# Kernel tuning notes

Hardware: AMD Instinct MI355X
Metric: run time of the kernel (lower is better)

## Reference

```python
import jax, jax.numpy as jnp
import numpy as np

B, T, E, H, FF = 8, 1024, 1024, 16, 4096
HD = E // H
SCALE = HD ** -0.5
EPS = 1e-12  # LayerNorm eps from TransformerLayer


def layer_norm(x, w, b):
    u = x.mean(-1, keepdims=True)
    s = ((x - u) ** 2).mean(-1, keepdims=True)  # biased variance, as in module
    return w * (x - u) / jnp.sqrt(s + EPS) + b


def setup_inputs() -> dict:
    key = jax.random.key(0)
    ks = jax.random.split(key, 8)
    std = 0.02  # nn.init.normal_(std=0.02)
    x = jax.random.normal(ks[0], (B, T, E), jnp.float32)
    # padding mask: positions >= length are padding (1 = ignore); ensure no all-masked row
    lengths = jax.random.randint(ks[1], (B,), T // 2, T + 1)
    self_padding_mask = jnp.arange(T)[None, :] >= lengths[:, None]
    # causal mask from SelfAttentionMask: triu(ones, 1)
    attn_mask = jnp.triu(jnp.ones((T, T), dtype=bool), 1)
    in_w = std * jax.random.normal(ks[2], (3 * E, E), jnp.float32)
    in_b = jnp.zeros((3 * E,), jnp.float32)
    out_w = std * jax.random.normal(ks[3], (E, E), jnp.float32)
    out_b = jnp.zeros((E,), jnp.float32)
    fc1_w = std * jax.random.normal(ks[4], (FF, E), jnp.float32)
    fc1_b = jnp.zeros((FF,), jnp.float32)
    fc2_w = std * jax.random.normal(ks[5], (E, FF), jnp.float32)
    fc2_b = jnp.zeros((E,), jnp.float32)
    ln1_w = jnp.ones((E,), jnp.float32)
    ln1_b = jnp.zeros((E,), jnp.float32)
    ln2_w = jnp.ones((E,), jnp.float32)
    ln2_b = jnp.zeros((E,), jnp.float32)
    return dict(x=x, in_w=in_w, in_b=in_b, out_w=out_w, out_b=out_b,
                fc1_w=fc1_w, fc1_b=fc1_b, fc2_w=fc2_w, fc2_b=fc2_b,
                ln1_w=ln1_w, ln1_b=ln1_b, ln2_w=ln2_w, ln2_b=ln2_b,
                self_padding_mask=self_padding_mask, attn_mask=attn_mask)


def reference(x, in_w, in_b, out_w, out_b, fc1_w, fc1_b, fc2_w, fc2_b,
              ln1_w, ln1_b, ln2_w, ln2_b, self_padding_mask, attn_mask):
    b, t, e = x.shape
    # --- self attention sublayer ---
    residual = x
    qkv = x @ in_w.T + in_b                       # [B,T,3E] fused in_proj (qkv_same path)
    q, k, v = jnp.split(qkv, 3, axis=-1)
    q = (q * SCALE).reshape(b, t, H, HD)
    k = k.reshape(b, t, H, HD)
    v = v.reshape(b, t, H, HD)
    scores = jnp.einsum('bqhd,bkhd->bhqk', q, k)  # [B,H,T,T]
    mask = attn_mask[None, None, :, :] | self_padding_mask[:, None, None, :]
    scores = jnp.where(mask, -jnp.inf, scores)
    p = jax.nn.softmax(scores, axis=-1)
    attn = jnp.einsum('bhqk,bkhd->bqhd', p, v).reshape(b, t, e)
    attn = attn @ out_w.T + out_b
    x = layer_norm(residual + attn, ln1_w, ln1_b)
    # --- feed-forward sublayer ---
    residual = x
    h = jax.nn.relu(x @ fc1_w.T + fc1_b)
    x = layer_norm(residual + (h @ fc2_w.T + fc2_b), ln2_w, ln2_b)
    return x
```

## Files before the change

kernel.cpp:

```cpp
#include <hip/hip_runtime.h>

typedef unsigned short u16;
typedef __attribute__((ext_vector_type(8))) short short8;
typedef __attribute__((ext_vector_type(4))) short short4v;
typedef __attribute__((ext_vector_type(4))) float f32x4;

#define DEV static __device__ __forceinline__

DEV float bf2f(u16 h) {
    union { unsigned int u; float f; } v; v.u = ((unsigned int)h) << 16; return v.f;
}
DEV u16 f2bf(float f) {
    union { float f; unsigned int u; } v; v.f = f;
    unsigned int r = (v.u + 0x7fff + ((v.u >> 16) & 1)) >> 16;
    return (u16)r;
}
DEV float ldx(const void* p, size_t i, int f32) {
    return f32 ? ((const float*)p)[i] : bf2f(((const u16*)p)[i]);
}

#define QSCL 0.18033688011112042f

#define GLD16(g, l) __builtin_amdgcn_global_load_lds( \
    (const __attribute__((address_space(1))) void*)(g), \
    (__attribute__((address_space(3))) void*)(l), 16, 0, 0)

#define STAGE(P, pf32, eoff, dst8) do {                                        \
    if (!(pf32)) { GLD16(((const u16*)(P)) + (eoff), (dst8)); }                \
    else {                                                                     \
        const float* _p = ((const float*)(P)) + (eoff);                        \
        f32x4 _a = *(const f32x4*)_p, _b = *(const f32x4*)(_p + 4);            \
        short8 _s;                                                             \
        _s[0]=(short)f2bf(_a[0]); _s[1]=(short)f2bf(_a[1]);                    \
        _s[2]=(short)f2bf(_a[2]); _s[3]=(short)f2bf(_a[3]);                    \
        _s[4]=(short)f2bf(_b[0]); _s[5]=(short)f2bf(_b[1]);                    \
        _s[6]=(short)f2bf(_b[2]); _s[7]=(short)f2bf(_b[3]);                    \
        *(short8*)(dst8) = _s;                                                 \
    } } while (0)

__global__ __launch_bounds__(64) void probe_kernel(
    const void* __restrict__ x, const void* __restrict__ pad,
    int* __restrict__ flags, int* __restrict__ flagsA)
{
    const int lane = threadIdx.x;
    const u16* xu = (const u16*)x;
    const unsigned int e = (xu[lane * 2] >> 7) & 0xFF;
    const int sane = (e >= 0x70 && e <= 0x8F) ? 1 : 0;
    unsigned long long m = __ballot(sane);
    const int f32 = (__popcll(m) < 32) ? 1 : 0;

    const unsigned int* pi = (const unsigned int*)pad;
    int bytes = 0;
#pragma unroll
    for (int j = 0; j < 6; j++) {
        unsigned int v = pi[128 + j * 64 + lane];
        if (v > 1u) bytes = 1;
    }
    m = __ballot(bytes);
    if (lane == 0) {
        flags[0] = f32; flags[1] = (m != 0ULL) ? 1 : 0;
        flagsA[0] = 0;  flagsA[1] = 0;
    }
}

__global__ __launch_bounds__(256) void conv8(
    const void* __restrict__ src, u16* __restrict__ dst, int n8,
    const int* __restrict__ flags)
{
    const int i = blockIdx.x * 256 + threadIdx.x;
    if (i >= n8) return;
    if (flags[0]) {
        const float* p = (const float*)src + (size_t)i * 8;
        f32x4 a = *(const f32x4*)p, b = *(const f32x4*)(p + 4);
        short8 s;
        s[0]=(short)f2bf(a[0]); s[1]=(short)f2bf(a[1]);
        s[2]=(short)f2bf(a[2]); s[3]=(short)f2bf(a[3]);
        s[4]=(short)f2bf(b[0]); s[5]=(short)f2bf(b[1]);
        s[6]=(short)f2bf(b[2]); s[7]=(short)f2bf(b[3]);
        ((short8*)dst)[i] = s;
    } else {
        ((short8*)dst)[i] = ((const short8*)src)[i];
    }
}

__global__ __launch_bounds__(256) void mask_to_bias(
    const void* __restrict__ pad, float* __restrict__ out,
    const int* __restrict__ flags)
{
    const int i = blockIdx.x * 256 + threadIdx.x;
    const int mv = flags[1] ? (int)((const unsigned char*)pad)[i]
                            : ((const int*)pad)[i];
    out[i] = mv ? -1e30f : 0.0f;
}

#define GEMM_CORE(Av, ASEL, a_row0, Wv, w_off, ldw, K)                        \
    __shared__ __align__(16) u16 As[128 * 32];                                \
    __shared__ __align__(16) u16 Bs[128 * 32];                                \
    const int inf32 = flags[0];                                               \
    const int af32  = (ASEL) ? inf32 : 0;                                     \
    const int tid  = threadIdx.x;                                             \
    const int lane = tid & 63;                                                \
    const int wave = tid >> 6;                                                \
    const int lc   = lane & 15;                                               \
    const int quad = lane >> 4;                                               \
    const int m0 = blockIdx.x * 128;                                          \
    const int n0 = blockIdx.y * 128;                                          \
    const int wm = (wave >> 1) * 64;                                          \
    const int wn = (wave & 1) * 64;                                           \
    const int r0 = tid >> 2;                                                  \
    const int ko = (tid & 3) * 8;                                             \
    f32x4 acc[4][4] = {};                                                     \
    for (int k0 = 0; k0 < (K); k0 += 32) {                                    \
        STAGE(Av, af32, ((size_t)(a_row0) + m0 + r0) * (K) + k0 + ko,         \
              &As[tid * 8]);                                                  \
        STAGE(Av, af32, ((size_t)(a_row0) + m0 + r0 + 64) * (K) + k0 + ko,    \
              &As[2048 + tid * 8]);                                           \
        STAGE(Wv, inf32, (size_t)(w_off) + (size_t)(n0 + r0) * (ldw) + k0 + ko,\
              &Bs[tid * 8]);                                                  \
        STAGE(Wv, inf32, (size_t)(w_off) + (size_t)(n0 + r0 + 64) * (ldw) + k0 + ko,\
              &Bs[2048 + tid * 8]);                                           \
        __syncthreads();                                                      \
        short8 afr[4], bfr[4];                                                \
        const int qd = quad * 8;                                              \
        _Pragma("unroll")                                                     \
        for (int mt = 0; mt < 4; mt++)                                        \
            afr[mt] = *(const short8*)&As[(wm + mt * 16 + lc) * 32 + qd];     \
        _Pragma("unroll")                                                     \
        for (int nt = 0; nt < 4; nt++)                                        \
            bfr[nt] = *(const short8*)&Bs[(wn + nt * 16 + lc) * 32 + qd];     \
        _Pragma("unroll")                                                     \
        for (int mt = 0; mt < 4; mt++)                                        \
            _Pragma("unroll")                                                 \
            for (int nt = 0; nt < 4; nt++)                                    \
                acc[mt][nt] = __builtin_amdgcn_mfma_f32_16x16x32_bf16(        \
                    afr[mt], bfr[nt], acc[mt][nt], 0, 0, 0);                  \
        __syncthreads();                                                      \
    }                                                                         \
    const int ce0 = n0 + wn + lc;                                             \
    const int re0 = m0 + wm + quad * 4;

template<int EPI>
__global__ __launch_bounds__(256, 2) void gemm_bt(
    const void* __restrict__ A, int a_sel, long a_row0,
    const void* __restrict__ W, long w_off,
    const void* __restrict__ bias, long b_off,
    const void* __restrict__ resid, int r_sel, long r_row0,
    u16* __restrict__ C, long c_row0,
    int N, int K, int ldw, const int* __restrict__ flags)
{
    GEMM_CORE(A, a_sel, a_row0, W, w_off, ldw, K)
    const int rf32 = r_sel ? inf32 : 0;
#pragma unroll
    for (int mt = 0; mt < 4; mt++) {
#pragma unroll
        for (int nt = 0; nt < 4; nt++) {
            const int c = ce0 + nt * 16;
            const float bv = ldx(bias, (size_t)b_off + c, inf32);
#pragma unroll
            for (int i = 0; i < 4; i++) {
                const int r = re0 + mt * 16 + i;
                float v = acc[mt][nt][i] + bv;
                if (EPI == 1)
                    v += ldx(resid, ((size_t)r_row0 + r) * N + c, rf32);
                if (EPI == 2) v = fmaxf(v, 0.0f);
                C[((size_t)c_row0 + r) * N + c] = f2bf(v);
            }
        }
    }
}

__global__ __launch_bounds__(256, 2) void gemm_qkv(
    const void* __restrict__ A, long a_row0,
    const void* __restrict__ W, const void* __restrict__ bias,
    u16* __restrict__ Qo, u16* __restrict__ Ko, u16* __restrict__ Vt,
    const int* __restrict__ flags)
{
    GEMM_CORE(A, 1, a_row0, W, 0, 1024, 1024)
    if (n0 < 1024) {
#pragma unroll
        for (int mt = 0; mt < 4; mt++)
#pragma unroll
            for (int nt = 0; nt < 4; nt++) {
                const int c = ce0 + nt * 16;
                const float bv = ldx(bias, c, inf32);
#pragma unroll
                for (int i = 0; i < 4; i++) {
                    const int r = re0 + mt * 16 + i;
                    Qo[((size_t)a_row0 + r) * 1024 + c] =
                        f2bf((acc[mt][nt][i] + bv) * QSCL);
                }
            }
    } else if (n0 < 2048) {
#pragma unroll
        for (int mt = 0; mt < 4; mt++)
#pragma unroll
            for (int nt = 0; nt < 4; nt++) {
                const int c = ce0 + nt * 16;
                const float bv = ldx(bias, c, inf32);
#pragma unroll
                for (int i = 0; i < 4; i++) {
                    const int r = re0 + mt * 16 + i;
                    Ko[(size_t)r * 1024 + (c - 1024)] = f2bf(acc[mt][nt][i] + bv);
                }
            }
    } else {
#pragma unroll
        for (int mt = 0; mt < 4; mt++)
#pragma unroll
            for (int nt = 0; nt < 4; nt++) {
                const int c = ce0 + nt * 16;
                const float bv = ldx(bias, c, inf32);
                const int cv = c - 2048;
                const int hh = cv >> 6, d = cv & 63;
                const int rb = re0 + mt * 16;
                const int bl = rb >> 10, t = rb & 1023;
                short4v pk;
#pragma unroll
                for (int i = 0; i < 4; i++)
                    pk[i] = (short)f2bf(acc[mt][nt][i] + bv);
                *(short4v*)&Vt[((size_t)(bl * 16 + hh) * 64 + d) * 1024 + t] = pk;
            }
    }
}

__global__ __launch_bounds__(256, 2) void gemm_accf32(
    const void* __restrict__ A, const void* __restrict__ W, long w_off,
    const void* __restrict__ bias, const u16* __restrict__ resid, long r_row0,
    float* __restrict__ C, int ldw, int init, const int* __restrict__ flags)
{
    GEMM_CORE(A, 0, 0, W, w_off, ldw, 1024)
#pragma unroll
    for (int mt = 0; mt < 4; mt++) {
#pragma unroll
        for (int nt = 0; nt < 4; nt++) {
            const int c = ce0 + nt * 16;
            const float bv = ldx(bias, c, inf32);
#pragma unroll
            for (int i = 0; i < 4; i++) {
                const int r = re0 + mt * 16 + i;
                float v = acc[mt][nt][i];
                if (init) v += bv + bf2f(resid[((size_t)r_row0 + r) * 1024 + c]);
                else      v += C[(size_t)r * 1024 + c];
                C[(size_t)r * 1024 + c] = v;
            }
        }
    }
}

#define GEMM8_PRE(Ag_, Wg_, Kg_)                                              \
    __shared__ __align__(16) u16 Ab[3][128 * 64];                             \
    __shared__ __align__(16) u16 Bb[3][256 * 64];                             \
    const u16* Ag = (Ag_); const u16* Wg = (Wg_); const int Kg = (Kg_);       \
    const int tid  = threadIdx.x;                                             \
    const int lane = tid & 63;                                                \
    const int lc   = lane & 15;                                               \
    const int quad = lane >> 4;                                               \
    const int w    = tid >> 6;                                                \
    const int wr   = w >> 2;                                                  \
    const int wc   = w & 3;                                                   \
    const int m0 = blockIdx.x * 128;                                          \
    const int n0 = blockIdx.y * 256;                                          \
    const int srow = tid >> 3;                                                \
    const int scol = (((tid & 7) ^ (srow & 7)) << 3);                         \
    const int sw0 = (((quad) ^ (lc & 7)) << 3);                               \
    const int sw1 = sw0 ^ 32;                                                 \
    f32x4 acc[4][4] = {};                                                     \
    short8 af[4], bf[4];

#define SA8(buf, kk) do {                                                     \
    GLD16(Ag + (size_t)(m0 + srow) * Kg + (kk) + scol, &Ab[buf][tid * 8]);    \
    GLD16(Ag + (size_t)(m0 + 64 + srow) * Kg + (kk) + scol,                   \
          &Ab[buf][4096 + tid * 8]); } while (0)
#define SB8a(buf, kk) do {                                                    \
    GLD16(Wg + (size_t)(n0 + srow) * Kg + (kk) + scol, &Bb[buf][tid * 8]);    \
    GLD16(Wg + (size_t)(n0 + 64 + srow) * Kg + (kk) + scol,                   \
          &Bb[buf][4096 + tid * 8]); } while (0)
#define SB8b(buf, kk) do {                                                    \
    GLD16(Wg + (size_t)(n0 + 128 + srow) * Kg + (kk) + scol,                  \
          &Bb[buf][8192 + tid * 8]);                                          \
    GLD16(Wg + (size_t)(n0 + 192 + srow) * Kg + (kk) + scol,                  \
          &Bb[buf][12288 + tid * 8]); } while (0)
#define LDFR(rbuf, SW) do { _Pragma("unroll")                                 \
    for (int q_ = 0; q_ < 4; q_++) {                                          \
        af[q_] = *(const short8*)&Ab[rbuf][(wr * 64 + q_ * 16 + lc) * 64 + (SW)];\
        bf[q_] = *(const short8*)&Bb[rbuf][(wc * 64 + q_ * 16 + lc) * 64 + (SW)];\
    } } while (0)
#define MFMA16 do { _Pragma("unroll")                                         \
    for (int mq = 0; mq < 4; mq++) { _Pragma("unroll")                        \
    for (int nq = 0; nq < 4; nq++)                                            \
        acc[mq][nq] = __builtin_amdgcn_mfma_f32_16x16x32_bf16(                \
            af[mq], bf[nq], acc[mq][nq], 0, 0, 0); } } while (0)

#define GEMM8_LOOP                                                            \
    const int NT = Kg >> 6;                                                   \
    SA8(0, 0); SB8a(0, 0); SB8b(0, 0);                                        \
    if (NT > 1) { SA8(1, 64); SB8a(1, 64); SB8b(1, 64); }                     \
    if (NT > 1) asm volatile("s_waitcnt vmcnt(6)" ::: "memory");              \
    else        asm volatile("s_waitcnt vmcnt(0)" ::: "memory");              \
    __builtin_amdgcn_s_barrier();                                             \
    int rb_ = 0, wb_ = 2;                                                     \
    for (int t = 0; t < NT; ++t) {                                            \
        const bool s_ = (t + 2 < NT);                                         \
        const int k2_ = (t + 2) << 6;                                         \
        LDFR(rb_, sw0);                                                       \
        if (s_) { SA8(wb_, k2_); SB8a(wb_, k2_); }                            \
        __builtin_amdgcn_s_barrier();                                         \
        asm volatile("s_waitcnt lgkmcnt(0)" ::: "memory");                    \
        __builtin_amdgcn_s_setprio(1);                                        \
        MFMA16;                                                               \
        __builtin_amdgcn_s_setprio(0);                                        \
        __builtin_amdgcn_s_barrier();                                         \
        LDFR(rb_, sw1);                                                       \
        if (s_) SB8b(wb_, k2_);                                               \
        __builtin_amdgcn_s_barrier();                                         \
        asm volatile("s_waitcnt lgkmcnt(0)" ::: "memory");                    \
        __builtin_amdgcn_s_setprio(1);                                        \
        MFMA16;                                                               \
        __builtin_amdgcn_s_setprio(0);                                        \
        if (s_) asm volatile("s_waitcnt vmcnt(6)" ::: "memory");              \
        else    asm volatile("s_waitcnt vmcnt(0)" ::: "memory");              \
        __builtin_amdgcn_s_barrier();                                         \
        rb_ = (rb_ == 2) ? 0 : rb_ + 1;                                      \
        wb_ = (wb_ == 2) ? 0 : wb_ + 1;                                      \
    }                                                                         \
    const int cb0 = n0 + wc * 64 + lc;                                        \
    const int rb0 = m0 + wr * 64 + quad * 4;

template<int EPI>
__global__ __launch_bounds__(512, 2) void gemm8(
    const u16* __restrict__ A, const u16* __restrict__ W,
    const u16* __restrict__ bias, const u16* __restrict__ resid,
    u16* __restrict__ C, int N, int K)
{
    GEMM8_PRE(A, W, K)
    GEMM8_LOOP
#pragma unroll
    for (int mq = 0; mq < 4; mq++) {
#pragma unroll
        for (int nq = 0; nq < 4; nq++) {
            const int cN = cb0 + nq * 16;
            const float bv = bf2f(bias[cN]);
#pragma unroll
            for (int i = 0; i < 4; i++) {
                const int rM = rb0 + mq * 16 + i;
                float v = acc[mq][nq][i] + bv;
                if (EPI == 1) v += bf2f(resid[(size_t)rM * N + cN]);
                if (EPI == 2) v = fmaxf(v, 0.0f);
                C[(size_t)rM * N + cN] = f2bf(v);
            }
        }
    }
}

__global__ __launch_bounds__(512, 2) void gemm8_qkv(
    const u16* __restrict__ A, const u16* __restrict__ W,
    const u16* __restrict__ bias,
    u16* __restrict__ Qo, u16* __restrict__ Ko, u16* __restrict__ Vt)
{
    GEMM8_PRE(A, W, 1024)
    GEMM8_LOOP
    if (n0 < 1024) {
#pragma unroll
        for (int mq = 0; mq < 4; mq++)
#pragma unroll
            for (int nq = 0; nq < 4; nq++) {
                const int c = cb0 + nq * 16;
                const float bv = bf2f(bias[c]);
#pragma unroll
                for (int i = 0; i < 4; i++) {
                    const int r = rb0 + mq * 16 + i;
                    Qo[(size_t)r * 1024 + c] =
                        f2bf((acc[mq][nq][i] + bv) * QSCL);
                }
            }
    } else if (n0 < 2048) {
#pragma unroll
        for (int mq = 0; mq < 4; mq++)
#pragma unroll
            for (int nq = 0; nq < 4; nq++) {
                const int c = cb0 + nq * 16;
                const float bv = bf2f(bias[c]);
#pragma unroll
                for (int i = 0; i < 4; i++) {
                    const int r = rb0 + mq * 16 + i;
                    Ko[(size_t)r * 1024 + (c - 1024)] =
                        f2bf(acc[mq][nq][i] + bv);
                }
            }
    } else {
#pragma unroll
        for (int mq = 0; mq < 4; mq++)
#pragma unroll
            for (int nq = 0; nq < 4; nq++) {
                const int c = cb0 + nq * 16;
                const float bv = bf2f(bias[c]);
                const int cv = c - 2048;
                const int hh = cv >> 6, d = cv & 63;
                const int rbase = rb0 + mq * 16;
                const int bl = rbase >> 10, tt = rbase & 1023;
                short4v pk;
#pragma unroll
                for (int i = 0; i < 4; i++)
                    pk[i] = (short)f2bf(acc[mq][nq][i] + bv);
                *(short4v*)&Vt[((size_t)(bl * 16 + hh) * 64 + d) * 1024 + tt] = pk;
            }
    }
}

#define GEMM256_PRE(Ag_, Wg_, Kg_)                                            \
    __shared__ __align__(16) u16 Ab2[2][2][8192];                             \
    __shared__ __align__(16) u16 Bb2[2][2][8192];                             \
    const u16* Ag = (Ag_); const u16* Wg = (Wg_); const int Kg = (Kg_);       \
    const int tid  = threadIdx.x;                                             \
    const int lane = tid & 63;                                                \
    const int lc   = lane & 15;                                               \
    const int quad = lane >> 4;                                               \
    const int w    = tid >> 6;                                                \
    const int wr   = w >> 2;                                                  \
    const int wc   = w & 3;                                                   \
    const int m0 = blockIdx.x * 256;                                          \
    const int n0 = blockIdx.y * 256;                                          \
    const int s_r = tid >> 2;                                                 \
    const int s_c = (((tid & 3) ^ ((tid >> 3) & 3)) << 3);                    \
    const int fsw = ((quad ^ ((lc >> 1) & 3)) << 3);                          \
    const int arow = wr * 128 + lc;                                           \
    const int brow = wc * 64 + lc;                                            \
    f32x4 acc[8][4] = {};                                                     \
    short8 af[4], bf[4];

#define SAH(buf, kk, tt) do {                                                 \
    GLD16(Ag + (size_t)(m0 + s_r) * Kg + (tt) * 64 + (kk) * 32 + s_c,         \
          &Ab2[buf][kk][tid * 8]);                                            \
    GLD16(Ag + (size_t)(m0 + 128 + s_r) * Kg + (tt) * 64 + (kk) * 32 + s_c,   \
          &Ab2[buf][kk][4096 + tid * 8]); } while (0)
#define SBH(buf, kk, tt) do {                                                 \
    GLD16(Wg + (size_t)(n0 + s_r) * Kg + (tt) * 64 + (kk) * 32 + s_c,         \
          &Bb2[buf][kk][tid * 8]);                                            \
    GLD16(Wg + (size_t)(n0 + 128 + s_r) * Kg + (tt) * 64 + (kk) * 32 + s_c,   \
          &Bb2[buf][kk][4096 + tid * 8]); } while (0)
#define LDA2(buf, kk, MH) do { _Pragma("unroll")                              \
    for (int q_ = 0; q_ < 4; q_++)                                            \
        af[q_] = *(const short8*)                                             \
            &Ab2[buf][kk][(arow + ((MH) * 4 + q_) * 16) * 32 + fsw]; } while (0)
#define LDB2(buf, kk) do { _Pragma("unroll")                                  \
    for (int q_ = 0; q_ < 4; q_++)                                            \
        bf[q_] = *(const short8*)                                             \
            &Bb2[buf][kk][(brow + q_ * 16) * 32 + fsw]; } while (0)
#define MF256(MH) do { _Pragma("unroll")                                      \
    for (int mq = 0; mq < 4; mq++) { _Pragma("unroll")                        \
    for (int nq = 0; nq < 4; nq++)                                            \
        acc[(MH) * 4 + mq][nq] = __builtin_amdgcn_mfma_f32_16x16x32_bf16(     \
            af[mq], bf[nq], acc[(MH) * 4 + mq][nq], 0, 0, 0); } } while (0)

#define GEMM256_LOOP                                                          \
    const int NT = Kg >> 6;                                                   \
    SAH(0, 0, 0); SBH(0, 0, 0); SAH(0, 1, 0); SBH(0, 1, 0);                   \
    if (NT > 1) SAH(1, 0, 1);                                                 \
    if (NT > 1) asm volatile("s_waitcnt vmcnt(2)" ::: "memory");              \
    else        asm volatile("s_waitcnt vmcnt(0)" ::: "memory");              \
    __builtin_amdgcn_s_barrier();                                             \
    for (int t = 0; t < NT; ++t) {                                            \
        const int c_ = t & 1, nx_ = c_ ^ 1;                                   \
        const bool s1_ = (t + 1 < NT), s2_ = (t + 2 < NT);                    \
                                                          \
        LDB2(c_, 0); LDA2(c_, 0, 0);                                          \
        if (s1_) SBH(nx_, 0, t + 1);                                          \
        __builtin_amdgcn_s_barrier();                                         \
        asm volatile("s_waitcnt lgkmcnt(0)" ::: "memory");                    \
        __builtin_amdgcn_s_setprio(1);                                        \
        MF256(0);                                                             \
        __builtin_amdgcn_s_setprio(0);                                        \
        __builtin_amdgcn_s_barrier();                                         \
                                         \
        LDA2(c_, 0, 1);                                                       \
        if (s1_) SAH(nx_, 1, t + 1);                                          \
        __builtin_amdgcn_s_barrier();                                         \
        asm volatile("s_waitcnt lgkmcnt(0)" ::: "memory");                    \
        __builtin_amdgcn_s_setprio(1);                                        \
        MF256(1);                                                             \
        __builtin_amdgcn_s_setprio(0);                                        \
        if (s1_) asm volatile("s_waitcnt vmcnt(6)" ::: "memory");             \
        else     asm volatile("s_waitcnt vmcnt(0)" ::: "memory");             \
        __builtin_amdgcn_s_barrier();                                         \
                                                          \
        LDB2(c_, 1); LDA2(c_, 1, 0);                                          \
        if (s1_) SBH(nx_, 1, t + 1);                                          \
        __builtin_amdgcn_s_barrier();                                         \
        asm volatile("s_waitcnt lgkmcnt(0)" ::: "memory");                    \
        __builtin_amdgcn_s_setprio(1);                                        \
        MF256(0);                                                             \
        __builtin_amdgcn_s_setprio(0);                                        \
        __builtin_amdgcn_s_barrier();                                         \
                \
        LDA2(c_, 1, 1);                                                       \
        if (s2_) SAH(c_, 0, t + 2);                                           \
        __builtin_amdgcn_s_barrier();                                         \
        asm volatile("s_waitcnt lgkmcnt(0)" ::: "memory");                    \
        __builtin_amdgcn_s_setprio(1);                                        \
        MF256(1);                                                             \
        __builtin_amdgcn_s_setprio(0);                                        \
        if (s2_)      asm volatile("s_waitcnt vmcnt(6)" ::: "memory");        \
        else if (s1_) asm volatile("s_waitcnt vmcnt(4)" ::: "memory");        \
        else          asm volatile("s_waitcnt vmcnt(0)" ::: "memory");        \
        __builtin_amdgcn_s_barrier();                                         \
    }                                                                         \
    const int cb0 = n0 + wc * 64 + lc;                                        \
    const int rb0 = m0 + wr * 128 + quad * 4;

template<int EPI>
__global__ __launch_bounds__(512, 2) void gemm256(
    const u16* __restrict__ A, const u16* __restrict__ W,
    const u16* __restrict__ bias, const u16* __restrict__ resid,
    u16* __restrict__ C, int N, int K)
{
    GEMM256_PRE(A, W, K)
    GEMM256_LOOP
#pragma unroll
    for (int mq = 0; mq < 8; mq++) {
#pragma unroll
        for (int nq = 0; nq < 4; nq++) {
            const int cN = cb0 + nq * 16;
            const float bv = bf2f(bias[cN]);
#pragma unroll
            for (int i = 0; i < 4; i++) {
                const int rM = rb0 + mq * 16 + i;
                float v = acc[mq][nq][i] + bv;
                if (EPI == 1) v += bf2f(resid[(size_t)rM * N + cN]);
                if (EPI == 2) v = fmaxf(v, 0.0f);
                C[(size_t)rM * N + cN] = f2bf(v);
            }
        }
    }
}

__global__ __launch_bounds__(256, 2) void attn_kernel(
    u16* __restrict__ QO, const u16* __restrict__ Ko,
    const u16* __restrict__ Vt, const float* __restrict__ kb, int b0)
{
    __shared__ __align__(16) u16 Qs[2 * 128 * 32];
    __shared__ __align__(16) u16 Ks[2][2 * 64 * 32];
    __shared__ __align__(16) u16 Vs[2][2 * 64 * 32];
    __shared__ __align__(16) u16 Ps[4][32 * 72];
    __shared__ float kba[1024];

    const int tid  = threadIdx.x;
    const int lane = tid & 63;
    const int w    = tid >> 6;
    const int lc   = lane & 15;
    const int quad = lane >> 4;
    const int bl = blockIdx.y >> 4;
    const int h  = blockIdx.y & 15;
    const int b  = b0 + bl;

    short8 bsum;
    {
        const short ov = (lc == 0) ? (short)0x3F80 : (short)0;
#pragma unroll
        for (int j = 0; j < 8; j++) bsum[j] = ov;
    }

    *(f32x4*)&kba[tid * 4] = *(const f32x4*)&kb[b * 1024 + tid * 4];

    for (int p = 0; p < 2; p++) {
        const int qt = p ? 7 - (int)blockIdx.x : (int)blockIdx.x;

#pragma unroll
        for (int it = 0; it < 4; it++) {
            const int kcd = it >> 1, half = it & 1;
            const int r = half * 64 + (tid >> 2);
            const int c = kcd * 32 + (tid & 3) * 8;
            GLD16(&QO[((size_t)(b * 1024 + qt * 128 + r)) * 1024 + h * 64 + c],
                  &Qs[kcd * 4096 + half * 2048 + tid * 8]);
        }
        {
            const int rr = tid >> 2;
#pragma unroll
            for (int it = 0; it < 2; it++) {
                const int cc = it * 32 + (tid & 3) * 8;
                GLD16(&Ko[((size_t)(bl * 1024 + rr)) * 1024 + h * 64 + cc],
                      &Ks[0][it * 2048 + tid * 8]);
                GLD16(&Vt[((size_t)(bl * 16 + h) * 64 + rr) * 1024 + cc],
                      &Vs[0][it * 2048 + tid * 8]);
            }
        }
        __syncthreads();

        short8 aq[2][2];
#pragma unroll
        for (int mt = 0; mt < 2; mt++)
#pragma unroll
            for (int kc = 0; kc < 2; kc++)
                aq[mt][kc] = *(const short8*)
                    &Qs[kc * 4096 + (w * 32 + mt * 16 + lc) * 32 + quad * 8];

        f32x4 o[2][4] = {};
        float m_i[2][4], l_i[2][4];
#pragma unroll
        for (int mt = 0; mt < 2; mt++)
#pragma unroll
            for (int i = 0; i < 4; i++) { m_i[mt][i] = -1e30f; l_i[mt][i] = 0.0f; }

        const int ktmax = 2 * qt + 2;
        for (int kt = 0; kt < ktmax; kt++) {
            const int cur = kt & 1;
            if (kt + 1 < ktmax) {
                const int nxt = cur ^ 1;
                const int rr = tid >> 2;
#pragma unroll
                for (int it = 0; it < 2; it++) {
                    const int cc = it * 32 + (tid & 3) * 8;
                    GLD16(&Ko[((size_t)(bl * 1024 + (kt + 1) * 64 + rr)) * 1024 + h * 64 + cc],
                          &Ks[nxt][it * 2048 + tid * 8]);
                    GLD16(&Vt[((size_t)(bl * 16 + h) * 64 + rr) * 1024 + (kt + 1) * 64 + cc],
                          &Vs[nxt][it * 2048 + tid * 8]);
                }
            }

            short8 bk[4][2];
#pragma unroll
            for (int nt = 0; nt < 4; nt++)
#pragma unroll
                for (int kc = 0; kc < 2; kc++)
                    bk[nt][kc] = *(const short8*)
                        &Ks[cur][kc * 2048 + (nt * 16 + lc) * 32 + quad * 8];

            f32x4 s[2][4];
#pragma unroll
            for (int mt = 0; mt < 2; mt++)
#pragma unroll
                for (int nt = 0; nt < 4; nt++) {
                    f32x4 z = {};
#pragma unroll
                    for (int kc = 0; kc < 2; kc++)
                        z = __builtin_amdgcn_mfma_f32_16x16x32_bf16(
                            aq[mt][kc], bk[nt][kc], z, 0, 0, 0);
                    s[mt][nt] = z;
                }

#pragma unroll
            for (int mt = 0; mt < 2; mt++)
#pragma unroll
                for (int nt = 0; nt < 4; nt++) {
                    const float kbv = kba[kt * 64 + nt * 16 + lc];
#pragma unroll
                    for (int i = 0; i < 4; i++) s[mt][nt][i] += kbv;
                }
            if (kt >= 2 * qt) {
#pragma unroll
                for (int mt = 0; mt < 2; mt++) {
                    const int qg0 = qt * 128 + w * 32 + mt * 16 + quad * 4;
#pragma unroll
                    for (int nt = 0; nt < 4; nt++) {
                        const int kg = kt * 64 + nt * 16 + lc;
#pragma unroll
                        for (int i = 0; i < 4; i++)
                            if (kg > qg0 + i) s[mt][nt][i] = -1e30f;
                    }
                }
            }

            float al[2][4];
#pragma unroll
            for (int mt = 0; mt < 2; mt++) {
                float mnew[4];
#pragma unroll
                for (int i = 0; i < 4; i++) {
                    float rm = fmaxf(fmaxf(s[mt][0][i], s[mt][1][i]),
                                     fmaxf(s[mt][2][i], s[mt][3][i]));
                    rm = fmaxf(rm, __shfl_xor(rm, 1));
                    rm = fmaxf(rm, __shfl_xor(rm, 2));
                    rm = fmaxf(rm, __shfl_xor(rm, 4));
                    rm = fmaxf(rm, __shfl_xor(rm, 8));
                    const float mn = fmaxf(m_i[mt][i], rm);
                    al[mt][i] = exp2f(m_i[mt][i] - mn);
                    m_i[mt][i] = mn;
                    mnew[i] = mn;
                }
#pragma unroll
                for (int nt = 0; nt < 4; nt++)
#pragma unroll
                    for (int i = 0; i < 4; i++)
                        s[mt][nt][i] = exp2f(s[mt][nt][i] - mnew[i]);
#pragma unroll
                for (int nt = 0; nt < 4; nt++) {
#pragma unroll
                    for (int i2 = 0; i2 < 2; i2++) {
                        unsigned int pk;
                        asm("v_cvt_pk_bf16_f32 %0, %1, %2"
                            : "=v"(pk)
                            : "v"(s[mt][nt][2 * i2]), "v"(s[mt][nt][2 * i2 + 1]));
                        Ps[w][(mt * 16 + quad * 4 + 2 * i2) * 72 + nt * 16 + lc] =
                            (u16)pk;
                        Ps[w][(mt * 16 + quad * 4 + 2 * i2 + 1) * 72 + nt * 16 + lc] =
                            (u16)(pk >> 16);
                    }
                }
            }
            int chg = 0;
#pragma unroll
            for (int mt = 0; mt < 2; mt++)
#pragma unroll
                for (int i = 0; i < 4; i++)
                    chg |= (al[mt][i] != 1.0f) ? 1 : 0;
            const int dor = __any(chg);

            short8 ap[2][2], bv2[4][2];
#pragma unroll
            for (int mt = 0; mt < 2; mt++)
#pragma unroll
                for (int kc = 0; kc < 2; kc++)
                    ap[mt][kc] = *(const short8*)
                        &Ps[w][(mt * 16 + lc) * 72 + kc * 32 + quad * 8];
#pragma unroll
            for (int nt = 0; nt < 4; nt++)
#pragma unroll
                for (int kc = 0; kc < 2; kc++)
                    bv2[nt][kc] = *(const short8*)
                        &Vs[cur][kc * 2048 + (nt * 16 + lc) * 32 + quad * 8];

            f32x4 ls[2] = {};
#pragma unroll
            for (int mt = 0; mt < 2; mt++)
#pragma unroll
                for (int kc = 0; kc < 2; kc++)
                    ls[mt] = __builtin_amdgcn_mfma_f32_16x16x32_bf16(
                        ap[mt][kc], bsum, ls[mt], 0, 0, 0);

#pragma unroll
            for (int mt = 0; mt < 2; mt++)
#pragma unroll
                for (int nt = 0; nt < 4; nt++) {
                    f32x4 oo = o[mt][nt];
                    if (dor) {
#pragma unroll
                        for (int i = 0; i < 4; i++) oo[i] *= al[mt][i];
                    }
#pragma unroll
                    for (int kc = 0; kc < 2; kc++)
                        oo = __builtin_amdgcn_mfma_f32_16x16x32_bf16(
                            ap[mt][kc], bv2[nt][kc], oo, 0, 0, 0);
                    o[mt][nt] = oo;
                }
#pragma unroll
            for (int mt = 0; mt < 2; mt++)
#pragma unroll
                for (int i = 0; i < 4; i++)
                    l_i[mt][i] = l_i[mt][i] * al[mt][i] + ls[mt][i];

            __syncthreads();
        }

#pragma unroll
        for (int mt = 0; mt < 2; mt++)
#pragma unroll
            for (int i = 0; i < 4; i++) {
                const float lv = __shfl(l_i[mt][i], (lane & 48));
                const float inv = lv > 0.0f ? 1.0f / lv : 0.0f;
#pragma unroll
                for (int nt = 0; nt < 4; nt++) {
                    const int r = qt * 128 + w * 32 + mt * 16 + quad * 4 + i;
                    const int d = nt * 16 + lc;
                    QO[((size_t)(b * 1024 + r)) * 1024 + h * 64 + d] =
                        f2bf(o[mt][nt][i] * inv);
                }
            }
    }
}

template<int IN16, int OUTSEL>
__global__ __launch_bounds__(256) void ln_kernel(
    const void* __restrict__ yv, const void* __restrict__ w,
    const void* __restrict__ bb, void* __restrict__ o, long o_row0,
    const int* __restrict__ flags)
{
    const int row = blockIdx.x;
    const int tid = threadIdx.x;
    const int inf32 = flags[0];
    float x0, x1, x2, x3;
    if (IN16) {
        const u16* p = (const u16*)yv + (size_t)row * 1024 + tid * 4;
        short4v v = *(const short4v*)p;
        x0 = bf2f((u16)v[0]); x1 = bf2f((u16)v[1]);
        x2 = bf2f((u16)v[2]); x3 = bf2f((u16)v[3]);
    } else {
        const float* p = (const float*)yv + (size_t)row * 1024 + tid * 4;
        f32x4 v = *(const f32x4*)p;
        x0 = v[0]; x1 = v[1]; x2 = v[2]; x3 = v[3];
    }
    float s = x0 + x1 + x2 + x3;
    float q = x0 * x0 + x1 * x1 + x2 * x2 + x3 * x3;
#pragma unroll
    for (int off = 32; off; off >>= 1) {
        s += __shfl_xor(s, off);
        q += __shfl_xor(q, off);
    }
    __shared__ float sm[8];
    const int lane = tid & 63, wv = tid >> 6;
    if (lane == 0) { sm[wv] = s; sm[4 + wv] = q; }
    __syncthreads();
    const float ts = sm[0] + sm[1] + sm[2] + sm[3];
    const float tq = sm[4] + sm[5] + sm[6] + sm[7];
    const float mean = ts * (1.0f / 1024.0f);
    float var = tq * (1.0f / 1024.0f) - mean * mean;
    if (var < 0.0f) var = 0.0f;
    const float rinv = rsqrtf(var + 1e-12f);

    const size_t obase = ((size_t)o_row0 + row) * 1024 + tid * 4;
#pragma unroll
    for (int j = 0; j < 4; j++) {
        const int c = tid * 4 + j;
        float xv = (j == 0) ? x0 : (j == 1) ? x1 : (j == 2) ? x2 : x3;
        float v = ldx(w, c, inf32) * ((xv - mean) * rinv) + ldx(bb, c, inf32);
        if (OUTSEL && inf32) ((float*)o)[obase + j] = v;
        else                 ((u16*)o)[obase + j] = f2bf(v);
    }
}

extern "C" void kernel_launch(void* const* d_in, const int* in_sizes, int n_in,
                              void* d_out, int out_size, void* d_ws, size_t ws_size,
                              hipStream_t stream)
{
    const void* x     = d_in[0];
    const void* in_w  = d_in[1];
    const void* in_b  = d_in[2];
    const void* out_w = d_in[3];
    const void* out_b = d_in[4];
    const void* fc1_w = d_in[5];
    const void* fc1_b = d_in[6];
    const void* fc2_w = d_in[7];
    const void* fc2_b = d_in[8];
    const void* ln1w  = d_in[9];
    const void* ln1b  = d_in[10];
    const void* ln2w  = d_in[11];
    const void* ln2b  = d_in[12];
    const void* pad   = d_in[13];
    u16* outp = (u16*)d_out;
    char* ws = (char*)d_ws;
    dim3 blk(256);
    dim3 blk8(512);

    const size_t MB = 1024 * 1024;
    const bool bigWS = ws_size >= (105 * MB + 64 * 1024);

    if (bigWS) {
        u16*   xb   = (u16*)(ws + 0);
        u16*   x1   = (u16*)(ws + 0);
        u16*   w1b  = (u16*)(ws + 16 * MB);
        u16*   wob  = (u16*)(ws + 22 * MB);
        u16*   f1b  = (u16*)(ws + 24 * MB);
        u16*   f2b  = (u16*)(ws + 32 * MB);
        u16*   inbb = (u16*)(ws + 40 * MB);
        u16*   outbb= (u16*)(ws + 40 * MB + 8192);
        u16*   f1bb = (u16*)(ws + 40 * MB + 16384);
        u16*   f2bb = (u16*)(ws + 40 * MB + 24576);
        u16*   Ko   = (u16*)(ws + 41 * MB);
        u16*   Vt   = (u16*)(ws + 57 * MB);
        u16*   y1   = (u16*)(ws + 73 * MB);
        u16*   h    = (u16*)(ws + 41 * MB);
        u16*   y2   = (u16*)(ws + 16 * MB);
        int*   flags  = (int*)(ws + 105 * MB);
        int*   flagsA = (int*)(ws + 105 * MB + 32);
        float* kbias  = (float*)(ws + 105 * MB + 64);

        probe_kernel<<<dim3(1), dim3(64), 0, stream>>>(x, pad, flags, flagsA);
        mask_to_bias<<<dim3(32), blk, 0, stream>>>(pad, kbias, flags);
        conv8<<<dim3(4096), blk, 0, stream>>>(x, xb, 1048576, flags);
        conv8<<<dim3(1536), blk, 0, stream>>>(in_w, w1b, 393216, flags);
        conv8<<<dim3(512),  blk, 0, stream>>>(out_w, wob, 131072, flags);
        conv8<<<dim3(2048), blk, 0, stream>>>(fc1_w, f1b, 524288, flags);
        conv8<<<dim3(2048), blk, 0, stream>>>(fc2_w, f2b, 524288, flags);
        conv8<<<dim3(2), blk, 0, stream>>>(in_b, inbb, 384, flags);
        conv8<<<dim3(1), blk, 0, stream>>>(out_b, outbb, 128, flags);
        conv8<<<dim3(2), blk, 0, stream>>>(fc1_b, f1bb, 512, flags);
        conv8<<<dim3(1), blk, 0, stream>>>(fc2_b, f2bb, 128, flags);

        gemm8_qkv<<<dim3(64, 12), blk8, 0, stream>>>(
            xb, w1b, inbb, outp, Ko, Vt);
        attn_kernel<<<dim3(4, 128), blk, 0, stream>>>(outp, Ko, Vt, kbias, 0);
        gemm8<1><<<dim3(64, 4), blk8, 0, stream>>>(
            outp, wob, outbb, xb, y1, 1024, 1024);
        ln_kernel<1, 0><<<dim3(8192), blk, 0, stream>>>(y1, ln1w, ln1b, x1, 0, flags);
        gemm256<2><<<dim3(32, 16), blk8, 0, stream>>>(
            x1, f1b, f1bb, nullptr, h, 4096, 1024);
        gemm8<1><<<dim3(64, 4), blk8, 0, stream>>>(
            h, f2b, f2bb, x1, y2, 1024, 4096);
        ln_kernel<1, 1><<<dim3(8192), blk, 0, stream>>>(y2, ln2w, ln2b, d_out, 0, flags);
    } else {
        u16*   Ko    = (u16*)(ws + 0);
        u16*   Vt    = (u16*)(ws + 4 * MB);
        u16*   y1h   = (u16*)(ws + 0);
        float* acc   = (float*)(ws + 0);
        u16*   hc    = (u16*)(ws + 8 * MB);
        int*   flags  = (int*)(ws + 12 * MB);
        int*   flagsA = (int*)(ws + 12 * MB + 32);
        float* kbias  = (float*)(ws + 12 * MB + 64);

        probe_kernel<<<dim3(1), dim3(64), 0, stream>>>(x, pad, flags, flagsA);
        mask_to_bias<<<dim3(32), blk, 0, stream>>>(pad, kbias, flags);

        for (int q = 0; q < 4; q++) {
            const long r0 = (long)q * 2048;
            gemm_qkv<<<dim3(16, 24), blk, 0, stream>>>(
                x, r0, in_w, in_b, outp, Ko, Vt, flags);
            attn_kernel<<<dim3(4, 32), blk, 0, stream>>>(
                outp, Ko, Vt, kbias, q * 2);
        }
        for (int hf = 0; hf < 2; hf++) {
            const long r0 = (long)hf * 4096;
            gemm_bt<1><<<dim3(32, 8), blk, 0, stream>>>(
                outp, 0, r0, out_w, 0, out_b, 0, x, 1, r0,
                y1h, 0, 1024, 1024, 1024, flags);
            ln_kernel<1, 0><<<dim3(4096), blk, 0, stream>>>(
                y1h, ln1w, ln1b, outp, r0, flags);
        }
        for (int q = 3; q >= 0; q--) {
            const long r0 = (long)q * 2048;
            for (int c = 0; c < 4; c++) {
                gemm_bt<2><<<dim3(16, 8), blk, 0, stream>>>(
                    outp, 0, r0, fc1_w, (long)c * 1024 * 1024, fc1_b, (long)c * 1024,
                    nullptr, 0, 0, hc, 0, 1024, 1024, 1024, flags);
                gemm_accf32<<<dim3(16, 8), blk, 0, stream>>>(
                    hc, fc2_w, (long)c * 1024, fc2_b, outp, r0,
                    acc, 4096, c == 0, flags);
            }
            ln_kernel<0, 1><<<dim3(2048), blk, 0, stream>>>(
                acc, ln2w, ln2b, d_out, r0, flags);
        }
    }
}
```

Before: 512.6 us.

## Fuse conversion launches and restructure gemm256 loop with fewer barriers

Nine separate conversion launches (input, weights, biases) are merged into one kernel that picks its source and destination by global index, which removes launch overhead. The gemm256 main loop now loads all A/B fragments for a K-tile up front into larger register arrays and interleaves global prefetches between MFMA groups. This cuts the per-tile barriers and lgkmcnt waits from about eight to two. The cost is higher register pressure from holding 24 short8 fragments, which may lower occupancy at launch_bounds(512,2). Dropping the intermediate barriers and explicit LDS waits also makes correct synchronisation depend on the compiler inserting the waits.

```diff
diff --git a/kernel.cpp b/kernel.cpp
--- a/kernel.cpp
+++ b/kernel.cpp
@@ -63,23 +63,40 @@
     }
 }
 
-__global__ __launch_bounds__(256) void conv8(
-    const void* __restrict__ src, u16* __restrict__ dst, int n8,
+__global__ __launch_bounds__(256) void conv_all(
+    const void* __restrict__ x, const void* __restrict__ in_w,
+    const void* __restrict__ out_w, const void* __restrict__ fc1_w,
+    const void* __restrict__ fc2_w, const void* __restrict__ in_b,
+    const void* __restrict__ out_b, const void* __restrict__ fc1_b,
+    const void* __restrict__ fc2_b,
+    u16* __restrict__ xb, u16* __restrict__ w1b, u16* __restrict__ wob,
+    u16* __restrict__ f1b, u16* __restrict__ f2b, u16* __restrict__ inbb,
+    u16* __restrict__ outbb, u16* __restrict__ f1bb, u16* __restrict__ f2bb,
     const int* __restrict__ flags)
 {
-    const int i = blockIdx.x * 256 + threadIdx.x;
-    if (i >= n8) return;
+    const size_t i = (size_t)blockIdx.x * 256 + threadIdx.x;
+    const void* src; u16* dst; size_t off;
+    if      (i < 1048576u) { src = x;     dst = xb;    off = i; }
+    else if (i < 1441792u) { src = in_w;  dst = w1b;   off = i - 1048576u; }
+    else if (i < 1572864u) { src = out_w; dst = wob;   off = i - 1441792u; }
+    else if (i < 2097152u) { src = fc1_w; dst = f1b;   off = i - 1572864u; }
+    else if (i < 2621440u) { src = fc2_w; dst = f2b;   off = i - 2097152u; }
+    else if (i < 2621824u) { src = in_b;  dst = inbb;  off = i - 2621440u; }
+    else if (i < 2621952u) { src = out_b; dst = outbb; off = i - 2621824u; }
+    else if (i < 2622464u) { src = fc1_b; dst = f1bb;  off = i - 2621952u; }
+    else if (i < 2622592u) { src = fc2_b; dst = f2bb;  off = i - 2622464u; }
+    else return;
     if (flags[0]) {
-        const float* p = (const float*)src + (size_t)i * 8;
+        const float* p = (const float*)src + off * 8;
         f32x4 a = *(const f32x4*)p, b = *(const f32x4*)(p + 4);
         short8 s;
         s[0]=(short)f2bf(a[0]); s[1]=(short)f2bf(a[1]);
         s[2]=(short)f2bf(a[2]); s[3]=(short)f2bf(a[3]);
         s[4]=(short)f2bf(b[0]); s[5]=(short)f2bf(b[1]);
         s[6]=(short)f2bf(b[2]); s[7]=(short)f2bf(b[3]);
-        ((short8*)dst)[i] = s;
+        ((short8*)dst)[off] = s;
     } else {
-        ((short8*)dst)[i] = ((const short8*)src)[i];
+        ((short8*)dst)[off] = ((const short8*)src)[off];
     }
 }
 
@@ -426,7 +443,8 @@
     const int arow = wr * 128 + lc;                                           \
     const int brow = wc * 64 + lc;                                            \
     f32x4 acc[8][4] = {};                                                     \
-    short8 af[4], bf[4];
+    short8 afx[4][4];                                                         \
+    short8 bfx[2][4];
 
 #define SAH(buf, kk, tt) do {                                                 \
     GLD16(Ag + (size_t)(m0 + s_r) * Kg + (tt) * 64 + (kk) * 32 + s_c,         \
@@ -438,19 +456,19 @@
           &Bb2[buf][kk][tid * 8]);                                            \
     GLD16(Wg + (size_t)(n0 + 128 + s_r) * Kg + (tt) * 64 + (kk) * 32 + s_c,   \
           &Bb2[buf][kk][4096 + tid * 8]); } while (0)
-#define LDA2(buf, kk, MH) do { _Pragma("unroll")                              \
+#define LDA3(DST, buf, kk, MH) do { _Pragma("unroll")                         \
     for (int q_ = 0; q_ < 4; q_++)                                            \
-        af[q_] = *(const short8*)                                             \
+        afx[DST][q_] = *(const short8*)                                       \
             &Ab2[buf][kk][(arow + ((MH) * 4 + q_) * 16) * 32 + fsw]; } while (0)
-#define LDB2(buf, kk) do { _Pragma("unroll")                                  \
+#define LDB3(DST, buf, kk) do { _Pragma("unroll")                             \
     for (int q_ = 0; q_ < 4; q_++)                                            \
-        bf[q_] = *(const short8*)                                             \
+        bfx[DST][q_] = *(const short8*)                                       \
             &Bb2[buf][kk][(brow + q_ * 16) * 32 + fsw]; } while (0)
-#define MF256(MH) do { _Pragma("unroll")                                      \
+#define MF3(AF, BF, MH) do { _Pragma("unroll")                                \
     for (int mq = 0; mq < 4; mq++) { _Pragma("unroll")                        \
     for (int nq = 0; nq < 4; nq++)                                            \
         acc[(MH) * 4 + mq][nq] = __builtin_amdgcn_mfma_f32_16x16x32_bf16(     \
-            af[mq], bf[nq], acc[(MH) * 4 + mq][nq], 0, 0, 0); } } while (0)
+            afx[AF][mq], bfx[BF][nq], acc[(MH) * 4 + mq][nq], 0, 0, 0); } } while (0)
 
 #define GEMM256_LOOP                                                          \
     const int NT = Kg >> 6;                                                   \
@@ -462,46 +480,30 @@
     for (int t = 0; t < NT; ++t) {                                            \
         const int c_ = t & 1, nx_ = c_ ^ 1;                                   \
         const bool s1_ = (t + 1 < NT), s2_ = (t + 2 < NT);                    \
-                                                          \
-        LDB2(c_, 0); LDA2(c_, 0, 0);                                          \
+                     \
+        LDB3(0, c_, 0); LDA3(0, c_, 0, 0);                                    \
+        LDA3(1, c_, 0, 1);                                                    \
+        LDB3(1, c_, 1); LDA3(2, c_, 1, 0);                                    \
+        LDA3(3, c_, 1, 1);                                                    \
         if (s1_) SBH(nx_, 0, t + 1);                                          \
-        __builtin_amdgcn_s_barrier();                                         \
-        asm volatile("s_waitcnt lgkmcnt(0)" ::: "memory");                    \
         __builtin_amdgcn_s_setprio(1);                                        \
-        MF256(0);                                                             \
+        MF3(0, 0, 0);                                                         \
         __builtin_amdgcn_s_setprio(0);                                        \
-        __builtin_amdgcn_s_barrier();                                         \
-                                         \
-        LDA2(c_, 0, 1);                                                       \
         if (s1_) SAH(nx_, 1, t + 1);                                          \
-        __builtin_amdgcn_s_barrier();                                         \
-        asm volatile("s_waitcnt lgkmcnt(0)" ::: "memory");                    \
         __builtin_amdgcn_s_setprio(1);                                        \
-        MF256(1);                                                             \
+        MF3(1, 0, 1);                                                         \
         __builtin_amdgcn_s_setprio(0);                                        \
-        if (s1_) asm volatile("s_waitcnt vmcnt(6)" ::: "memory");             \
+        __builtin_amdgcn_s_barrier();       \
+        if (s1_) SBH(nx_, 1, t + 1);                                          \
+        __builtin_amdgcn_s_setprio(1);                                        \
+        MF3(2, 1, 0);                                                         \
+        __builtin_amdgcn_s_setprio(0);                                        \
+        if (s2_) SAH(c_, 0, t + 2);                                           \
+        __builtin_amdgcn_s_setprio(1);                                        \
+        MF3(3, 1, 1);                                                         \
+        __builtin_amdgcn_s_setprio(0);                                        \
+        if (s2_) asm volatile("s_waitcnt vmcnt(2)" ::: "memory");             \
         else     asm volatile("s_waitcnt vmcnt(0)" ::: "memory");             \
-        __builtin_amdgcn_s_barrier();                                         \
-                                                          \
-        LDB2(c_, 1); LDA2(c_, 1, 0);                                          \
-        if (s1_) SBH(nx_, 1, t + 1);                                          \
-        __builtin_amdgcn_s_barrier();                                         \
-        asm volatile("s_waitcnt lgkmcnt(0)" ::: "memory");                    \
-        __builtin_amdgcn_s_setprio(1);                                        \
-        MF256(0);                                                             \
-        __builtin_amdgcn_s_setprio(0);                                        \
-        __builtin_amdgcn_s_barrier();                                         \
-                \
-        LDA2(c_, 1, 1);                                                       \
-        if (s2_) SAH(c_, 0, t + 2);                                           \
-        __builtin_amdgcn_s_barrier();                                         \
-        asm volatile("s_waitcnt lgkmcnt(0)" ::: "memory");                    \
-        __builtin_amdgcn_s_setprio(1);                                        \
-        MF256(1);                                                             \
-        __builtin_amdgcn_s_setprio(0);                                        \
-        if (s2_)      asm volatile("s_waitcnt vmcnt(6)" ::: "memory");        \
-        else if (s1_) asm volatile("s_waitcnt vmcnt(4)" ::: "memory");        \
-        else          asm volatile("s_waitcnt vmcnt(0)" ::: "memory");        \
         __builtin_amdgcn_s_barrier();                                         \
     }                                                                         \
     const int cb0 = n0 + wc * 64 + lc;                                        \
@@ -864,15 +866,9 @@
 
         probe_kernel<<<dim3(1), dim3(64), 0, stream>>>(x, pad, flags, flagsA);
         mask_to_bias<<<dim3(32), blk, 0, stream>>>(pad, kbias, flags);
-        conv8<<<dim3(4096), blk, 0, stream>>>(x, xb, 1048576, flags);
-        conv8<<<dim3(1536), blk, 0, stream>>>(in_w, w1b, 393216, flags);
-        conv8<<<dim3(512),  blk, 0, stream>>>(out_w, wob, 131072, flags);
-        conv8<<<dim3(2048), blk, 0, stream>>>(fc1_w, f1b, 524288, flags);
-        conv8<<<dim3(2048), blk, 0, stream>>>(fc2_w, f2b, 524288, flags);
-        conv8<<<dim3(2), blk, 0, stream>>>(in_b, inbb, 384, flags);
-        conv8<<<dim3(1), blk, 0, stream>>>(out_b, outbb, 128, flags);
-        conv8<<<dim3(2), blk, 0, stream>>>(fc1_b, f1bb, 512, flags);
-        conv8<<<dim3(1), blk, 0, stream>>>(fc2_b, f2bb, 128, flags);
+        conv_all<<<dim3(10245), blk, 0, stream>>>(
+            x, in_w, out_w, fc1_w, fc2_w, in_b, out_b, fc1_b, fc2_b,
+            xb, w1b, wob, f1b, f2b, inbb, outbb, f1bb, f2bb, flags);
 
         gemm8_qkv<<<dim3(64, 12), blk8, 0, stream>>>(
             xb, w1b, inbb, outp, Ko, Vt);
```

After: 499.9 us. 2.5% less time.
